# Kernel optimization log

Hardware: AMD Instinct MI355X
Metric: run time of the kernel (lower is better)

Reference implementation:

```python
import jax, jax.numpy as jnp
import numpy as np

D_BINS = 59          # cfg.cam_d
BEV_H, BEV_W = 128, 128


def setup_inputs() -> dict:
    key = jax.random.key(0)
    k = jax.random.split(key, 7)
    B, N, Cin, H, W = 4, 6, 256, 16, 44
    C = 80  # cfg.cam_bev_c
    img_feats = jax.random.normal(k[0], (B, N, Cin, H, W), dtype=jnp.float32)
    rots = jax.random.normal(k[1], (B, N, 3, 3), dtype=jnp.float32)
    trans = jax.random.normal(k[2], (B, N, 3), dtype=jnp.float32)
    intrins = jax.random.normal(k[3], (B, N, 3, 3), dtype=jnp.float32)
    # 1x1 conv == per-pixel linear layer: weight (D+C, Cin), bias (D+C,)
    w_depth = jax.random.normal(k[4], (D_BINS + C, Cin), dtype=jnp.float32) / np.sqrt(Cin)
    b_depth = jnp.zeros((D_BINS + C,), dtype=jnp.float32)
    # projected BEV grid indices (what get_geometry produces via randint)
    geom = jax.random.randint(k[5], (B, N, D_BINS, H, W, 2), 0, BEV_H, dtype=jnp.int32)
    return {"img_feats": img_feats, "rots": rots, "trans": trans,
            "intrins": intrins, "w_depth": w_depth, "b_depth": b_depth,
            "geom": geom}


def reference(img_feats, rots, trans, intrins, w_depth, b_depth, geom):
    B, N, Cin, H, W = img_feats.shape
    C = w_depth.shape[0] - D_BINS
    # depth_net: 1x1 conv -> (B, N, D+C, H, W)
    x = jnp.einsum('bnchw,oc->bnohw', img_feats, w_depth) + b_depth[None, None, :, None, None]
    depth = jax.nn.softmax(x[:, :, :D_BINS], axis=2)          # (B,N,D,H,W)
    context = x[:, :, D_BINS:]                                 # (B,N,C,H,W)
    # outer product: (B,N,D,C,H,W) -> (B,N,D,H,W,C)
    frustum = depth[:, :, :, None] * context[:, :, None]
    frustum = jnp.transpose(frustum, (0, 1, 2, 4, 5, 3))
    # voxel pooling: scatter-add frustum points into BEV grid by geom indices
    cell = geom[..., 0] * BEV_W + geom[..., 1]                 # (B,N,D,H,W)
    flat_idx = (jnp.arange(B, dtype=jnp.int32)[:, None] * (BEV_H * BEV_W)
                + cell.reshape(B, -1)).reshape(-1)
    bev = jax.ops.segment_sum(frustum.reshape(-1, C), flat_idx,
                              num_segments=B * BEV_H * BEV_W)
    return bev.reshape(B, BEV_H, BEV_W, C).transpose(0, 3, 1, 2)  # (B,C,bev_h,bev_w)
```

## Files before the change

kernel.cpp:

```cpp
#include <hip/hip_runtime.h>
#include <hip/hip_bf16.h>
#include <math.h>

#define D_BINS 59
#define CTX    80
#define O_TOT  139
#define K_CIN  256
#define PIXELS 704
#define BNPAIR 24
#define BEVHW  16384
#define NBATCH 4
#define NPOINT (BNPAIR * D_BINS * PIXELS)
#define NPIX   (BNPAIR * PIXELS)

#define NTILE   128
#define NBUCKET (NBATCH * NTILE)
#define TCELLS  128

#define PIXB    128
#define NBLK    (NPIX / PIXB)
#define EPB     (PIXB * D_BINS)

#define CAP     2816
#define CAPP    (CAP + TCELLS * 7)

#define XDEPTH_OFF 0
#define CTX_OFF    (XDEPTH_OFF + NPOINT)
#define CNTMAT_OFF (CTX_OFF + BNPAIR * PIXELS * CTX)
#define OFSMAT_OFF (CNTMAT_OFF + NBLK * NBUCKET)
#define PLIST_OFF  (OFSMAT_OFF + NBLK * NBUCKET)

__global__ __launch_bounds__(256) void gemm_kernel(
    const float* __restrict__ img,
    const float* __restrict__ w,
    const float* __restrict__ bias,
    float* __restrict__ xdepth,
    __hip_bfloat16* __restrict__ ctx)
{
    __shared__ float As[16][64];
    __shared__ float Bs[16][64];

    const int tid = threadIdx.x;
    const int tx  = tid & 15;
    const int ty  = tid >> 4;
    const int bn  = blockIdx.z;
    const int o0  = blockIdx.y * 64;
    const int p0  = blockIdx.x * 64;

    const float* imgbn = img + (size_t)bn * K_CIN * PIXELS;

    float acc[4][4];
#pragma unroll
    for (int i = 0; i < 4; ++i)
#pragma unroll
        for (int j = 0; j < 4; ++j) acc[i][j] = 0.f;

    const int a_ol = tid >> 2;
    const int a_kc = (tid & 3) * 4;
    const int b_kl = tid >> 4;
    const int b_p4 = (tid & 15) * 4;

    for (int kt = 0; kt < K_CIN; kt += 16) {
        {
            const int o = o0 + a_ol;
            float4 v = make_float4(0.f, 0.f, 0.f, 0.f);
            if (o < O_TOT) v = *(const float4*)&w[(size_t)o * K_CIN + kt + a_kc];
            As[a_kc + 0][a_ol] = v.x;
            As[a_kc + 1][a_ol] = v.y;
            As[a_kc + 2][a_ol] = v.z;
            As[a_kc + 3][a_ol] = v.w;
        }
        *(float4*)&Bs[b_kl][b_p4] =
            *(const float4*)&imgbn[(size_t)(kt + b_kl) * PIXELS + p0 + b_p4];
        __syncthreads();

#pragma unroll
        for (int kk = 0; kk < 16; ++kk) {
            const float4 a = *(const float4*)&As[kk][ty * 4];
            const float4 b = *(const float4*)&Bs[kk][tx * 4];
            const float av[4] = {a.x, a.y, a.z, a.w};
            const float bv[4] = {b.x, b.y, b.z, b.w};
#pragma unroll
            for (int i = 0; i < 4; ++i)
#pragma unroll
                for (int j = 0; j < 4; ++j)
                    acc[i][j] += av[i] * bv[j];
        }
        __syncthreads();
    }

#pragma unroll
    for (int i = 0; i < 4; ++i) {
        const int o = o0 + ty * 4 + i;
        if (o >= O_TOT) continue;
        const float bv = bias[o];
        if (o < D_BINS) {
            float4 r = make_float4(acc[i][0] + bv, acc[i][1] + bv,
                                   acc[i][2] + bv, acc[i][3] + bv);
            *(float4*)&xdepth[((size_t)bn * D_BINS + o) * PIXELS + p0 + tx * 4] = r;
        } else {
            const int c = o - D_BINS;
            __hip_bfloat16* dst = ctx + ((size_t)bn * PIXELS + p0 + tx * 4) * CTX + c;
#pragma unroll
            for (int j = 0; j < 4; ++j)
                dst[(size_t)j * CTX] = __float2bfloat16(acc[i][j] + bv);
        }
    }
}

__global__ __launch_bounds__(256) void fill_kernel(
    const float* __restrict__ xdepth,
    const int*   __restrict__ geom,
    uint2*       __restrict__ plist,
    int*         __restrict__ cntmat,
    int*         __restrict__ ofsmat)
{
    __shared__ unsigned short cache[D_BINS][PIXB];
    __shared__ float red[2][PIXB];
    __shared__ int lh[NBUCKET];
    __shared__ int lofs[NBUCKET];
    __shared__ int lcur[NBUCKET];
    __shared__ int s[256];

    const int tid = threadIdx.x;
    const int px  = tid & (PIXB - 1);
    const int h   = tid >> 7;
    const int pix = blockIdx.x * PIXB + px;
    const int bn  = pix / PIXELS;
    const int pp  = pix - bn * PIXELS;
    const int b   = bn / 6;
    const int d0  = h * 30;

    if (tid < NBUCKET) { lh[tid] = 0; lh[tid + 256] = 0; }
    __syncthreads();

    const float* base = xdepth + (size_t)bn * D_BINS * PIXELS + pp;
    float v[30];
    float lm = -INFINITY;
#pragma unroll
    for (int i = 0; i < 30; ++i) {
        const int d = d0 + i;
        v[i] = (d < D_BINS) ? base[(size_t)d * PIXELS] : -INFINITY;
        lm = fmaxf(lm, v[i]);
    }
    red[h][px] = lm;
    __syncthreads();
    const float gm = fmaxf(red[0][px], red[1][px]);
    __syncthreads();
    float ls = 0.f;
#pragma unroll
    for (int i = 0; i < 30; ++i) {
        v[i] = __expf(v[i] - gm);
        ls += v[i];
    }
    red[h][px] = ls;
    __syncthreads();
    const float inv = 1.f / (red[0][px] + red[1][px]);
#pragma unroll
    for (int i = 0; i < 30; ++i) v[i] *= inv;

    const int2* g2 = (const int2*)geom;
#pragma unroll
    for (int i = 0; i < 30; ++i) {
        const int d = d0 + i;
        if (d < D_BINS) {
            const int2 g = g2[((size_t)(bn * D_BINS + d)) * PIXELS + pp];
            const int bucket = b * NTILE + (g.x >> 3) * 8 + (g.y >> 4);
            const int cell   = (g.x & 7) * 16 + (g.y & 15);
            cache[d][px] = (unsigned short)((bucket << 7) | cell);
            atomicAdd(&lh[bucket], 1);
        }
    }
    __syncthreads();

    const int v0 = lh[2 * tid];
    const int v1 = lh[2 * tid + 1];
    const int p  = v0 + v1;
    s[tid] = p;
    __syncthreads();
#pragma unroll
    for (int off = 1; off < 256; off <<= 1) {
        int t = (tid >= off) ? s[tid - off] : 0;
        __syncthreads();
        s[tid] += t;
        __syncthreads();
    }
    const int excl = s[tid] - p;
    lofs[2 * tid]     = excl;
    lofs[2 * tid + 1] = excl + v0;
    lcur[2 * tid]     = 0;
    lcur[2 * tid + 1] = 0;
    cntmat[(size_t)blockIdx.x * NBUCKET + 2 * tid]     = v0;
    cntmat[(size_t)blockIdx.x * NBUCKET + 2 * tid + 1] = v1;
    ofsmat[(size_t)blockIdx.x * NBUCKET + 2 * tid]     = excl;
    ofsmat[(size_t)blockIdx.x * NBUCKET + 2 * tid + 1] = excl + v0;
    __syncthreads();

    uint2* dst = plist + (size_t)blockIdx.x * EPB;
    const unsigned ctxoff = (unsigned)((bn * PIXELS + pp) * CTX);
#pragma unroll
    for (int i = 0; i < 30; ++i) {
        const int d = d0 + i;
        if (d < D_BINS) {
            const unsigned u = cache[d][px];
            const int bucket = (int)(u >> 7);
            const int pos = lofs[bucket] + atomicAdd(&lcur[bucket], 1);
            dst[pos] = make_uint2(__float_as_uint(v[i]), (ctxoff << 7) | (u & 127u));
        }
    }
}

__global__ __launch_bounds__(1024) void gather_kernel(
    const uint2* __restrict__ plist,
    const int*   __restrict__ cntmat,
    const int*   __restrict__ ofsmat,
    const unsigned short* __restrict__ ctx,
    float*       __restrict__ out)
{
    __shared__ float sacc[CTX][TCELLS + 1];
    __shared__ uint2 bufB[CAPP];
    __shared__ int sg[256];
    __shared__ int segcnt[NBLK], segofs[NBLK];
    __shared__ int cellcnt[TCELLS], celloff[TCELLS], cellcur[TCELLS], sc[TCELLS];
    uint2* bufA = (uint2*)sacc;

    const int tid    = threadIdx.x;
    const int wv     = tid >> 6;
    const int lane   = tid & 63;
    const int bucket = blockIdx.x;

    if (tid < 256) {
        const int c = (tid < NBLK) ? cntmat[(size_t)tid * NBUCKET + bucket] : 0;
        sg[tid] = c;
        if (tid < NBLK) segcnt[tid] = c;
    }
    __syncthreads();
#pragma unroll
    for (int off = 1; off < 256; off <<= 1) {
        int t = (tid < 256 && tid >= off) ? sg[tid - off] : 0;
        __syncthreads();
        if (tid < 256) sg[tid] += t;
        __syncthreads();
    }
    if (tid < NBLK) segofs[tid] = sg[tid] - segcnt[tid];
    __syncthreads();
    const int total = sg[255];

    for (int blk = wv; blk < NBLK; blk += 16) {
        const int n = segcnt[blk];
        if (!n) continue;
        const int dstb = segofs[blk];
        const uint2* sp = plist + (size_t)blk * EPB + ofsmat[(size_t)blk * NBUCKET + bucket];
        for (int i = lane; i < n; i += 64) {
            const int d = dstb + i;
            if (d < CAP) bufA[d] = sp[i];
        }
    }
    const int ncap = (total < CAP) ? total : CAP;
    __syncthreads();

    if (tid < TCELLS) cellcnt[tid] = 0;
    __syncthreads();
    for (int i = tid; i < ncap; i += 1024)
        atomicAdd(&cellcnt[bufA[i].y & 127u], 1);
    __syncthreads();
    if (tid < TCELLS) sc[tid] = (cellcnt[tid] + 7) & ~7;
    __syncthreads();
#pragma unroll
    for (int off = 1; off < TCELLS; off <<= 1) {
        int t = (tid < TCELLS && tid >= off) ? sc[tid - off] : 0;
        __syncthreads();
        if (tid < TCELLS) sc[tid] += t;
        __syncthreads();
    }
    if (tid < TCELLS) {
        celloff[tid] = sc[tid] - ((cellcnt[tid] + 7) & ~7);
        cellcur[tid] = 0;
    }
    __syncthreads();
    const int padtotal = sc[TCELLS - 1];
    for (int i = tid; i < padtotal; i += 1024) bufB[i] = make_uint2(0u, 0u);
    __syncthreads();
    for (int i = tid; i < ncap; i += 1024) {
        const uint2 e = bufA[i];
        const int c = (int)(e.y & 127u);
        bufB[celloff[c] + atomicAdd(&cellcur[c], 1)] = e;
    }
    __syncthreads();

    for (int c = wv; c < TCELLS; c += 16) {
        const int s0 = celloff[c];
        const int pc = (cellcnt[c] + 7) & ~7;
        float a0 = 0.f, a1 = 0.f;
        for (int i = 0; i < pc; i += 8) {
            uint2 e[8];
#pragma unroll
            for (int r = 0; r < 8; ++r) e[r] = bufB[s0 + i + r];
            if (lane < 40) {
                unsigned u[8];
#pragma unroll
                for (int r = 0; r < 8; ++r)
                    u[r] = *(const unsigned*)(ctx + (e[r].y >> 7) + 2 * lane);
#pragma unroll
                for (int r = 0; r < 8; ++r) {
                    const float d  = __uint_as_float(e[r].x);
                    const float f0 = __uint_as_float(u[r] << 16);
                    const float f1 = __uint_as_float(u[r] & 0xffff0000u);
                    a0 += d * f0;
                    a1 += d * f1;
                }
            }
        }
        if (lane < 40) {
            sacc[2 * lane][c]     = a0;
            sacc[2 * lane + 1][c] = a1;
        }
    }

    if (total > CAP) {
        for (int blk = 0; blk < NBLK; ++blk) {
            const int dstb = segofs[blk];
            const int n    = segcnt[blk];
            if (dstb + n <= CAP) continue;
            const uint2* sp = plist + (size_t)blk * EPB + ofsmat[(size_t)blk * NBUCKET + bucket];
            const int i0 = (CAP > dstb) ? (CAP - dstb) : 0;
            for (int i = i0; i < n; ++i) {
                const uint2 e = sp[i];
                const int c = (int)(e.y & 127u);
                if ((c & 15) == wv && lane < 40) {
                    const unsigned u = *(const unsigned*)(ctx + (e.y >> 7) + 2 * lane);
                    const float dep = __uint_as_float(e.x);
                    sacc[2 * lane][c]     += dep * __uint_as_float(u << 16);
                    sacc[2 * lane + 1][c] += dep * __uint_as_float(u & 0xffff0000u);
                }
            }
        }
    }
    __syncthreads();

    const int b  = bucket >> 7;
    const int tl = bucket & 127;
    const int tr = tl >> 3;
    const int tc = tl & 7;
    const int c0  = tid >> 4;
    const int col = tid & 15;
#pragma unroll
    for (int cc = c0; cc < CTX; cc += 64) {
#pragma unroll
        for (int r = 0; r < 8; ++r) {
            out[((size_t)(b * CTX + cc)) * BEVHW + (tr * 8 + r) * 128 + tc * 16 + col]
                = sacc[cc][r * 16 + col];
        }
    }
}

extern "C" void kernel_launch(void* const* d_in, const int* in_sizes, int n_in,
                              void* d_out, int out_size, void* d_ws, size_t ws_size,
                              hipStream_t stream)
{
    const float* img  = (const float*)d_in[0];
    const float* w    = (const float*)d_in[4];
    const float* bias = (const float*)d_in[5];
    const int*   geom = (const int*)d_in[6];
    float*       out  = (float*)d_out;

    float* ws     = (float*)d_ws;
    float* xdepth = ws + XDEPTH_OFF;
    __hip_bfloat16* ctx = (__hip_bfloat16*)(ws + CTX_OFF);
    int*   cntmat = (int*)(ws + CNTMAT_OFF);
    int*   ofsmat = (int*)(ws + OFSMAT_OFF);
    uint2* plist  = (uint2*)(ws + PLIST_OFF);

    {
        dim3 grid(11, 3, BNPAIR);
        gemm_kernel<<<grid, 256, 0, stream>>>(img, w, bias, xdepth, ctx);
    }
    fill_kernel<<<NBLK, 256, 0, stream>>>(xdepth, geom, plist, cntmat, ofsmat);

    gather_kernel<<<NBUCKET, 1024, 0, stream>>>(plist, cntmat, ofsmat,
                                                (const unsigned short*)ctx, out);
}
```

Measured before the change: 157.1 us.

## Fuse depth GEMM with softmax and bucket fill, shrink pixel tiles to 32

Merges the 1x1-conv GEMM and the softmax/bucketing fill kernel into one kernel per 32-pixel tile. Depth logits now stay in shared memory instead of making a global round trip. This also drops one launch and raises the fill block count from 132 to 528, so the gather kernel must scan 528 segments per bucket. To handle that, its prefix scan widens to 1024 threads and segment copies are spread over 4-lane groups. The trade-offs are more segments per bucket in the gather, smaller contiguous copy runs, and every block re-reading all 139 weight rows.

```diff
diff --git a/kernel.cpp b/kernel.cpp
--- a/kernel.cpp
+++ b/kernel.cpp
@@ -10,202 +10,198 @@
 #define BNPAIR 24
 #define BEVHW  16384
 #define NBATCH 4
-#define NPOINT (BNPAIR * D_BINS * PIXELS)
 #define NPIX   (BNPAIR * PIXELS)
 
 #define NTILE   128
 #define NBUCKET (NBATCH * NTILE)
 #define TCELLS  128
 
-#define PIXB    128
-#define NBLK    (NPIX / PIXB)
-#define EPB     (PIXB * D_BINS)
+#define PTILE   32
+#define NPT     (PIXELS / PTILE)
+#define NBLK    (NPT * BNPAIR)
+#define EPB     (PTILE * D_BINS)
 
 #define CAP     2816
 #define CAPP    (CAP + TCELLS * 7)
 
-#define XDEPTH_OFF 0
-#define CTX_OFF    (XDEPTH_OFF + NPOINT)
-#define CNTMAT_OFF (CTX_OFF + BNPAIR * PIXELS * CTX)
+#define CTX_OFF    0
+#define CNTMAT_OFF (CTX_OFF + (NPIX * CTX) / 2)
 #define OFSMAT_OFF (CNTMAT_OFF + NBLK * NBUCKET)
 #define PLIST_OFF  (OFSMAT_OFF + NBLK * NBUCKET)
 
-__global__ __launch_bounds__(256) void gemm_kernel(
+__global__ __launch_bounds__(256) void fused_kernel(
     const float* __restrict__ img,
     const float* __restrict__ w,
     const float* __restrict__ bias,
-    float* __restrict__ xdepth,
-    __hip_bfloat16* __restrict__ ctx)
-{
-    __shared__ float As[16][64];
-    __shared__ float Bs[16][64];
-
-    const int tid = threadIdx.x;
-    const int tx  = tid & 15;
-    const int ty  = tid >> 4;
-    const int bn  = blockIdx.z;
-    const int o0  = blockIdx.y * 64;
-    const int p0  = blockIdx.x * 64;
-
-    const float* imgbn = img + (size_t)bn * K_CIN * PIXELS;
-
-    float acc[4][4];
-#pragma unroll
-    for (int i = 0; i < 4; ++i)
-#pragma unroll
-        for (int j = 0; j < 4; ++j) acc[i][j] = 0.f;
-
-    const int a_ol = tid >> 2;
-    const int a_kc = (tid & 3) * 4;
-    const int b_kl = tid >> 4;
-    const int b_p4 = (tid & 15) * 4;
-
-    for (int kt = 0; kt < K_CIN; kt += 16) {
-        {
-            const int o = o0 + a_ol;
-            float4 v = make_float4(0.f, 0.f, 0.f, 0.f);
-            if (o < O_TOT) v = *(const float4*)&w[(size_t)o * K_CIN + kt + a_kc];
-            As[a_kc + 0][a_ol] = v.x;
-            As[a_kc + 1][a_ol] = v.y;
-            As[a_kc + 2][a_ol] = v.z;
-            As[a_kc + 3][a_ol] = v.w;
-        }
-        *(float4*)&Bs[b_kl][b_p4] =
-            *(const float4*)&imgbn[(size_t)(kt + b_kl) * PIXELS + p0 + b_p4];
-        __syncthreads();
-
-#pragma unroll
-        for (int kk = 0; kk < 16; ++kk) {
-            const float4 a = *(const float4*)&As[kk][ty * 4];
-            const float4 b = *(const float4*)&Bs[kk][tx * 4];
-            const float av[4] = {a.x, a.y, a.z, a.w};
-            const float bv[4] = {b.x, b.y, b.z, b.w};
-#pragma unroll
-            for (int i = 0; i < 4; ++i)
-#pragma unroll
-                for (int j = 0; j < 4; ++j)
-                    acc[i][j] += av[i] * bv[j];
-        }
-        __syncthreads();
-    }
-
-#pragma unroll
-    for (int i = 0; i < 4; ++i) {
-        const int o = o0 + ty * 4 + i;
-        if (o >= O_TOT) continue;
-        const float bv = bias[o];
-        if (o < D_BINS) {
-            float4 r = make_float4(acc[i][0] + bv, acc[i][1] + bv,
-                                   acc[i][2] + bv, acc[i][3] + bv);
-            *(float4*)&xdepth[((size_t)bn * D_BINS + o) * PIXELS + p0 + tx * 4] = r;
-        } else {
-            const int c = o - D_BINS;
-            __hip_bfloat16* dst = ctx + ((size_t)bn * PIXELS + p0 + tx * 4) * CTX + c;
-#pragma unroll
-            for (int j = 0; j < 4; ++j)
-                dst[(size_t)j * CTX] = __float2bfloat16(acc[i][j] + bv);
-        }
-    }
-}
-
-__global__ __launch_bounds__(256) void fill_kernel(
-    const float* __restrict__ xdepth,
     const int*   __restrict__ geom,
+    __hip_bfloat16* __restrict__ ctx,
     uint2*       __restrict__ plist,
     int*         __restrict__ cntmat,
     int*         __restrict__ ofsmat)
 {
-    __shared__ unsigned short cache[D_BINS][PIXB];
-    __shared__ float red[2][PIXB];
-    __shared__ int lh[NBUCKET];
-    __shared__ int lofs[NBUCKET];
-    __shared__ int lcur[NBUCKET];
-    __shared__ int s[256];
+    __shared__ union {
+        struct { float As[16][161]; float Bs[16][32]; } p1;
+        struct {
+            float L[D_BINS][PTILE + 1];
+            float red[8][PTILE];
+            int lh[NBUCKET], lofs[NBUCKET], lcur[NBUCKET];
+            int s[256];
+        } p2;
+    } sm;
 
     const int tid = threadIdx.x;
-    const int px  = tid & (PIXB - 1);
-    const int h   = tid >> 7;
-    const int pix = blockIdx.x * PIXB + px;
-    const int bn  = pix / PIXELS;
-    const int pp  = pix - bn * PIXELS;
+    const int pt  = blockIdx.x;
+    const int bn  = blockIdx.y;
+    const int p0  = pt * PTILE;
+    const int blk = bn * NPT + pt;
     const int b   = bn / 6;
-    const int d0  = h * 30;
-
-    if (tid < NBUCKET) { lh[tid] = 0; lh[tid + 256] = 0; }
-    __syncthreads();
-
-    const float* base = xdepth + (size_t)bn * D_BINS * PIXELS + pp;
-    float v[30];
+
+    const int tx = tid & 7;
+    const int ty = tid >> 3;
+    const float* imgbn = img + (size_t)bn * K_CIN * PIXELS;
+
+    float acc[5][4];
+#pragma unroll
+    for (int i = 0; i < 5; ++i)
+#pragma unroll
+        for (int j = 0; j < 4; ++j) acc[i][j] = 0.f;
+
+    for (int kt = 0; kt < K_CIN; kt += 16) {
+        for (int e = tid; e < O_TOT * 4; e += 256) {
+            const int o  = e >> 2;
+            const int kc = (e & 3) * 4;
+            const float4 v = *(const float4*)&w[(size_t)o * K_CIN + kt + kc];
+            sm.p1.As[kc + 0][o] = v.x;
+            sm.p1.As[kc + 1][o] = v.y;
+            sm.p1.As[kc + 2][o] = v.z;
+            sm.p1.As[kc + 3][o] = v.w;
+        }
+        if (tid < 128) {
+            const int kl = tid >> 3;
+            const int p4 = (tid & 7) * 4;
+            *(float4*)&sm.p1.Bs[kl][p4] =
+                *(const float4*)&imgbn[(size_t)(kt + kl) * PIXELS + p0 + p4];
+        }
+        __syncthreads();
+
+#pragma unroll
+        for (int kk = 0; kk < 16; ++kk) {
+            const float4 b4 = *(const float4*)&sm.p1.Bs[kk][tx * 4];
+            const float bv4[4] = {b4.x, b4.y, b4.z, b4.w};
+            float av[5];
+#pragma unroll
+            for (int i = 0; i < 5; ++i) av[i] = sm.p1.As[kk][ty * 5 + i];
+#pragma unroll
+            for (int i = 0; i < 5; ++i)
+#pragma unroll
+                for (int j = 0; j < 4; ++j)
+                    acc[i][j] += av[i] * bv4[j];
+        }
+        __syncthreads();
+    }
+
+#pragma unroll
+    for (int i = 0; i < 5; ++i) {
+        const int o = ty * 5 + i;
+        if (o >= O_TOT) continue;
+        const float bv = bias[o];
+        if (o < D_BINS) {
+#pragma unroll
+            for (int j = 0; j < 4; ++j)
+                sm.p2.L[o][tx * 4 + j] = acc[i][j] + bv;
+        } else {
+            const int c = o - D_BINS;
+            __hip_bfloat16* dst = ctx + ((size_t)bn * PIXELS + p0 + tx * 4) * CTX + c;
+#pragma unroll
+            for (int j = 0; j < 4; ++j)
+                dst[(size_t)j * CTX] = __float2bfloat16(acc[i][j] + bv);
+        }
+    }
+    sm.p2.lh[tid] = 0;
+    sm.p2.lh[tid + 256] = 0;
+    __syncthreads();
+
+    const int px = tid & (PTILE - 1);
+    const int h  = tid >> 5;
+    const int d0 = h * 8;
+    float v[8];
     float lm = -INFINITY;
 #pragma unroll
-    for (int i = 0; i < 30; ++i) {
+    for (int i = 0; i < 8; ++i) {
         const int d = d0 + i;
-        v[i] = (d < D_BINS) ? base[(size_t)d * PIXELS] : -INFINITY;
+        v[i] = (d < D_BINS) ? sm.p2.L[d][px] : -INFINITY;
         lm = fmaxf(lm, v[i]);
     }
-    red[h][px] = lm;
-    __syncthreads();
-    const float gm = fmaxf(red[0][px], red[1][px]);
+    sm.p2.red[h][px] = lm;
+    __syncthreads();
+    float gm = sm.p2.red[0][px];
+#pragma unroll
+    for (int hh = 1; hh < 8; ++hh) gm = fmaxf(gm, sm.p2.red[hh][px]);
     __syncthreads();
     float ls = 0.f;
 #pragma unroll
-    for (int i = 0; i < 30; ++i) {
+    for (int i = 0; i < 8; ++i) {
         v[i] = __expf(v[i] - gm);
         ls += v[i];
     }
-    red[h][px] = ls;
-    __syncthreads();
-    const float inv = 1.f / (red[0][px] + red[1][px]);
-#pragma unroll
-    for (int i = 0; i < 30; ++i) v[i] *= inv;
-
+    sm.p2.red[h][px] = ls;
+    __syncthreads();
+    float tot = 0.f;
+#pragma unroll
+    for (int hh = 0; hh < 8; ++hh) tot += sm.p2.red[hh][px];
+    const float inv = 1.f / tot;
+#pragma unroll
+    for (int i = 0; i < 8; ++i) v[i] *= inv;
+
+    const int pp = p0 + px;
     const int2* g2 = (const int2*)geom;
-#pragma unroll
-    for (int i = 0; i < 30; ++i) {
+    unsigned uu[8];
+#pragma unroll
+    for (int i = 0; i < 8; ++i) {
         const int d = d0 + i;
         if (d < D_BINS) {
             const int2 g = g2[((size_t)(bn * D_BINS + d)) * PIXELS + pp];
             const int bucket = b * NTILE + (g.x >> 3) * 8 + (g.y >> 4);
             const int cell   = (g.x & 7) * 16 + (g.y & 15);
-            cache[d][px] = (unsigned short)((bucket << 7) | cell);
-            atomicAdd(&lh[bucket], 1);
-        }
-    }
-    __syncthreads();
-
-    const int v0 = lh[2 * tid];
-    const int v1 = lh[2 * tid + 1];
-    const int p  = v0 + v1;
-    s[tid] = p;
+            uu[i] = (unsigned)((bucket << 7) | cell);
+            atomicAdd(&sm.p2.lh[bucket], 1);
+        }
+    }
+    __syncthreads();
+
+    const int v0 = sm.p2.lh[2 * tid];
+    const int v1 = sm.p2.lh[2 * tid + 1];
+    const int pr = v0 + v1;
+    sm.p2.s[tid] = pr;
     __syncthreads();
 #pragma unroll
     for (int off = 1; off < 256; off <<= 1) {
-        int t = (tid >= off) ? s[tid - off] : 0;
-        __syncthreads();
-        s[tid] += t;
-        __syncthreads();
-    }
-    const int excl = s[tid] - p;
-    lofs[2 * tid]     = excl;
-    lofs[2 * tid + 1] = excl + v0;
-    lcur[2 * tid]     = 0;
-    lcur[2 * tid + 1] = 0;
-    cntmat[(size_t)blockIdx.x * NBUCKET + 2 * tid]     = v0;
-    cntmat[(size_t)blockIdx.x * NBUCKET + 2 * tid + 1] = v1;
-    ofsmat[(size_t)blockIdx.x * NBUCKET + 2 * tid]     = excl;
-    ofsmat[(size_t)blockIdx.x * NBUCKET + 2 * tid + 1] = excl + v0;
-    __syncthreads();
-
-    uint2* dst = plist + (size_t)blockIdx.x * EPB;
+        int t = (tid >= off) ? sm.p2.s[tid - off] : 0;
+        __syncthreads();
+        sm.p2.s[tid] += t;
+        __syncthreads();
+    }
+    const int excl = sm.p2.s[tid] - pr;
+    sm.p2.lofs[2 * tid]     = excl;
+    sm.p2.lofs[2 * tid + 1] = excl + v0;
+    sm.p2.lcur[2 * tid]     = 0;
+    sm.p2.lcur[2 * tid + 1] = 0;
+    cntmat[(size_t)blk * NBUCKET + 2 * tid]     = v0;
+    cntmat[(size_t)blk * NBUCKET + 2 * tid + 1] = v1;
+    ofsmat[(size_t)blk * NBUCKET + 2 * tid]     = excl;
+    ofsmat[(size_t)blk * NBUCKET + 2 * tid + 1] = excl + v0;
+    __syncthreads();
+
+    uint2* dst = plist + (size_t)blk * EPB;
     const unsigned ctxoff = (unsigned)((bn * PIXELS + pp) * CTX);
 #pragma unroll
-    for (int i = 0; i < 30; ++i) {
+    for (int i = 0; i < 8; ++i) {
         const int d = d0 + i;
         if (d < D_BINS) {
-            const unsigned u = cache[d][px];
-            const int bucket = (int)(u >> 7);
-            const int pos = lofs[bucket] + atomicAdd(&lcur[bucket], 1);
-            dst[pos] = make_uint2(__float_as_uint(v[i]), (ctxoff << 7) | (u & 127u));
+            const int bkt = (int)(uu[i] >> 7);
+            const int pos = sm.p2.lofs[bkt] + atomicAdd(&sm.p2.lcur[bkt], 1);
+            dst[pos] = make_uint2(__float_as_uint(v[i]),
+                                  (ctxoff << 7) | (uu[i] & 127u));
         }
     }
 }
@@ -219,41 +215,46 @@
 {
     __shared__ float sacc[CTX][TCELLS + 1];
     __shared__ uint2 bufB[CAPP];
-    __shared__ int sg[256];
     __shared__ int segcnt[NBLK], segofs[NBLK];
     __shared__ int cellcnt[TCELLS], celloff[TCELLS], cellcur[TCELLS], sc[TCELLS];
     uint2* bufA = (uint2*)sacc;
+    int*   sg   = (int*)bufB;
 
     const int tid    = threadIdx.x;
     const int wv     = tid >> 6;
     const int lane   = tid & 63;
     const int bucket = blockIdx.x;
 
-    if (tid < 256) {
+    {
         const int c = (tid < NBLK) ? cntmat[(size_t)tid * NBUCKET + bucket] : 0;
         sg[tid] = c;
         if (tid < NBLK) segcnt[tid] = c;
     }
     __syncthreads();
 #pragma unroll
-    for (int off = 1; off < 256; off <<= 1) {
-        int t = (tid < 256 && tid >= off) ? sg[tid - off] : 0;
-        __syncthreads();
-        if (tid < 256) sg[tid] += t;
+    for (int off = 1; off < 1024; off <<= 1) {
+        int t = (tid >= off) ? sg[tid - off] : 0;
+        __syncthreads();
+        sg[tid] += t;
         __syncthreads();
     }
     if (tid < NBLK) segofs[tid] = sg[tid] - segcnt[tid];
-    __syncthreads();
-    const int total = sg[255];
-
-    for (int blk = wv; blk < NBLK; blk += 16) {
-        const int n = segcnt[blk];
-        if (!n) continue;
-        const int dstb = segofs[blk];
-        const uint2* sp = plist + (size_t)blk * EPB + ofsmat[(size_t)blk * NBUCKET + bucket];
-        for (int i = lane; i < n; i += 64) {
-            const int d = dstb + i;
-            if (d < CAP) bufA[d] = sp[i];
+    const int total = sg[1023];
+    __syncthreads();
+
+    {
+        const int grp = lane >> 2;
+        const int sub = lane & 3;
+        for (int s = wv * 16 + grp; s < NBLK; s += 256) {
+            const int n = segcnt[s];
+            if (!n) continue;
+            const int dstb = segofs[s];
+            const uint2* sp = plist + (size_t)s * EPB
+                            + ofsmat[(size_t)s * NBUCKET + bucket];
+            for (int i = sub; i < n; i += 4) {
+                const int d = dstb + i;
+                if (d < CAP) bufA[d] = sp[i];
+            }
         }
     }
     const int ncap = (total < CAP) ? total : CAP;
@@ -304,10 +305,8 @@
 #pragma unroll
                 for (int r = 0; r < 8; ++r) {
                     const float d  = __uint_as_float(e[r].x);
-                    const float f0 = __uint_as_float(u[r] << 16);
-                    const float f1 = __uint_as_float(u[r] & 0xffff0000u);
-                    a0 += d * f0;
-                    a1 += d * f1;
+                    a0 += d * __uint_as_float(u[r] << 16);
+                    a1 += d * __uint_as_float(u[r] & 0xffff0000u);
                 }
             }
         }
@@ -322,7 +321,8 @@
             const int dstb = segofs[blk];
             const int n    = segcnt[blk];
             if (dstb + n <= CAP) continue;
-            const uint2* sp = plist + (size_t)blk * EPB + ofsmat[(size_t)blk * NBUCKET + bucket];
+            const uint2* sp = plist + (size_t)blk * EPB
+                            + ofsmat[(size_t)blk * NBUCKET + bucket];
             const int i0 = (CAP > dstb) ? (CAP - dstb) : 0;
             for (int i = i0; i < n; ++i) {
                 const uint2 e = sp[i];
@@ -365,18 +365,16 @@
     float*       out  = (float*)d_out;
 
     float* ws     = (float*)d_ws;
-    float* xdepth = ws + XDEPTH_OFF;
     __hip_bfloat16* ctx = (__hip_bfloat16*)(ws + CTX_OFF);
     int*   cntmat = (int*)(ws + CNTMAT_OFF);
     int*   ofsmat = (int*)(ws + OFSMAT_OFF);
     uint2* plist  = (uint2*)(ws + PLIST_OFF);
 
     {
-        dim3 grid(11, 3, BNPAIR);
-        gemm_kernel<<<grid, 256, 0, stream>>>(img, w, bias, xdepth, ctx);
-    }
-    fill_kernel<<<NBLK, 256, 0, stream>>>(xdepth, geom, plist, cntmat, ofsmat);
-
+        dim3 grid(NPT, BNPAIR);
+        fused_kernel<<<grid, 256, 0, stream>>>(img, w, bias, geom,
+                                               ctx, plist, cntmat, ofsmat);
+    }
     gather_kernel<<<NBUCKET, 1024, 0, stream>>>(plist, cntmat, ofsmat,
                                                 (const unsigned short*)ctx, out);
 }
```

After: 159.6 us. Within noise of the previous version (+1.6%).
